# Kernel tuning notes

Hardware: AMD Instinct MI355X
Metric: run time of the kernel (lower is better)

## Reference

```python
import jax, jax.numpy as jnp
import numpy as np

B, T, IN, H, L = 8192, 200, 4, 16, 4
MLP_IN, MLP_HID, MLP_OUT = H * T, 64, IN * 7


def _lstm_layer(x, Wih, Whh, b):
    """x: [B,T,Din]; Wih: [4H,Din]; Whh: [4H,H]; b: [4H]. Returns [B,T,H].
    PyTorch gate order: i, f, g, o."""
    xg = jnp.einsum('btd,gd->btg', x, Wih) + b  # precompute input projections [B,T,4H]
    h0 = jnp.zeros((x.shape[0], H), x.dtype)
    c0 = jnp.zeros((x.shape[0], H), x.dtype)

    def step(carry, xt):
        h, c = carry
        gates = xt + h @ Whh.T  # [B,4H]
        i, f, g, o = jnp.split(gates, 4, axis=-1)
        i = jax.nn.sigmoid(i); f = jax.nn.sigmoid(f)
        g = jnp.tanh(g); o = jax.nn.sigmoid(o)
        c = f * c + i * g
        h = o * jnp.tanh(c)
        return (h, c), h

    _, hs = jax.lax.scan(step, (h0, c0), jnp.swapaxes(xg, 0, 1))  # [T,B,H]
    return jnp.swapaxes(hs, 0, 1)


def setup_inputs() -> dict:
    key = jax.random.key(0)
    ks = jax.random.split(key, 12)
    s = 1.0 / np.sqrt(H)
    u = lambda k, shp: jax.random.uniform(k, shp, jnp.float32, -s, s)
    x = jax.random.normal(ks[0], (B, T, IN), jnp.float32)
    Wih0 = u(ks[1], (4 * H, IN))            # layer 0 input weights
    Wih_rest = u(ks[2], (L - 1, 4 * H, H))  # layers 1..3
    Whh = u(ks[3], (L, 4 * H, H))
    bih = u(ks[4], (L, 4 * H))
    bhh = u(ks[5], (L, 4 * H))
    sm = 1.0 / np.sqrt(MLP_IN)
    W1 = jax.random.uniform(ks[6], (MLP_HID, MLP_IN), jnp.float32, -sm, sm)
    b1 = jax.random.uniform(ks[7], (MLP_HID,), jnp.float32, -sm, sm)
    sm2 = 1.0 / np.sqrt(MLP_HID)
    W2 = jax.random.uniform(ks[8], (MLP_OUT, MLP_HID), jnp.float32, -sm2, sm2)
    b2 = jax.random.uniform(ks[9], (MLP_OUT,), jnp.float32, -sm2, sm2)
    return {"x": x, "Wih0": Wih0, "Wih_rest": Wih_rest, "Whh": Whh,
            "bih": bih, "bhh": bhh, "W1": W1, "b1": b1, "W2": W2, "b2": b2}


def reference(x, Wih0, Wih_rest, Whh, bih, bhh, W1, b1, W2, b2):
    h = _lstm_layer(x, Wih0, Whh[0], bih[0] + bhh[0])
    for l in range(1, L):
        h = _lstm_layer(h, Wih_rest[l - 1], Whh[l], bih[l] + bhh[l])
    flat = h.reshape(-1, H * T)  # [B, 3200]
    hid = jax.nn.relu(flat @ W1.T + b1)
    return hid @ W2.T + b2  # [B, 28]
```

## Files before the change

### kernel.cpp

```cpp
#include <hip/hip_runtime.h>
#include <hip/hip_bf16.h>


typedef short  bf16x8 __attribute__((ext_vector_type(8)));
typedef float  f32x4  __attribute__((ext_vector_type(4)));

namespace {
constexpr int kT     = 200;
constexpr int kOut   = 28;
constexpr int kSteps = kT + 4;
constexpr float kNLog2e  = -1.4426950408889634f;
constexpr float kN2Log2e = -2.8853900817779268f;
constexpr int kW1Elems = 64 * 3200;
}

union FragU { bf16x8 v; unsigned u[4]; };

__device__ __forceinline__ float fast_rcp(float v){ return __builtin_amdgcn_rcpf(v); }
__device__ __forceinline__ float fast_exp2(float v){ return __builtin_amdgcn_exp2f(v); }
__device__ __forceinline__ float sig_scaled(float p){ return fast_rcp(1.0f + fast_exp2(p)); }
__device__ __forceinline__ float tanh_true(float v){
  return fmaf(fast_rcp(1.0f + fast_exp2(kN2Log2e*v)), 2.0f, -1.0f);
}

__device__ __forceinline__ void split8(const float* v, FragU& hi, FragU& lo){
#pragma unroll
  for (int r=0;r<4;++r){
    unsigned ua=__float_as_uint(v[2*r]), ub=__float_as_uint(v[2*r+1]);
    hi.u[r] = (ua>>16) | (ub & 0xffff0000u);
    float af=__uint_as_float(ua & 0xffff0000u);
    float bf=__uint_as_float(ub & 0xffff0000u);
    float al=v[2*r]-af, bl=v[2*r+1]-bf;
    lo.u[r] = (__float_as_uint(al)>>16) | (__float_as_uint(bl) & 0xffff0000u);
  }
}

__global__ __launch_bounds__(256)
void presplit_w1(const float* __restrict__ W1,
                 short* __restrict__ W1h, short* __restrict__ W1l){
  int i = blockIdx.x*256 + threadIdx.x;
  if (i < kW1Elems){
    float v = W1[i];
    unsigned u = __float_as_uint(v);
    float hif = __uint_as_float(u & 0xffff0000u);
    float lo  = v - hif;
    W1h[i] = (short)(u >> 16);
    W1l[i] = (short)(__float_as_uint(lo) >> 16);
  }
}

template<bool PS>
__global__ __launch_bounds__(256)
void lstm_pipe(const float* __restrict__ x,
               const float* __restrict__ Wih0,
               const float* __restrict__ Wihr,
               const float* __restrict__ Whh,
               const float* __restrict__ bih,
               const float* __restrict__ bhh,
               const float* __restrict__ W1,
               const float* __restrict__ b1,
               const float* __restrict__ W2,
               const float* __restrict__ b2,
               const short* __restrict__ W1h,
               const short* __restrict__ W1l,
               float* __restrict__ out)
{
  __shared__ float ldsH[2][4][16][16];
  __shared__ float ldsR[16][68];

  const int tid  = threadIdx.x;
  const int lane = tid & 63;
  const int wv   = tid >> 6;
  const int s    = lane & 15;
  const int q    = lane >> 4;
  const int l    = wv;
  const int sbase = blockIdx.x * 16;

  for (int i = tid; i < 2*4*16*16; i += 256) ((float*)ldsH)[i] = 0.f;

  FragU A[4][2];
#pragma unroll
  for (int tile=0;tile<4;++tile){
    const int grow = tile*16 + s;
    const float kE = (tile==2)? kN2Log2e : kNLog2e;
    float v[8];
    if (l==0){
#pragma unroll
      for (int e=0;e<8;++e){
        float w = 0.f;
        if (q==0 && e<4) w = Wih0[grow*4+e];
        if (q>=2)        w = Whh[grow*16 + (q&1)*8 + e];
        v[e] = w*kE;
      }
    } else {
#pragma unroll
      for (int e=0;e<8;++e){
        float w = (q<2) ? Wihr[((l-1)*64+grow)*16 + q*8 + e]
                        : Whh [(( l )*64+grow)*16 + (q&1)*8 + e];
        v[e] = w*kE;
      }
    }
    split8(v, A[tile][0], A[tile][1]);
  }

  f32x4 biasf[4];
#pragma unroll
  for (int tile=0;tile<4;++tile){
    const float kE = (tile==2)? kN2Log2e : kNLog2e;
#pragma unroll
    for (int r=0;r<4;++r){
      const int row = l*64 + tile*16 + 4*q + r;
      biasf[tile][r] = (bih[row] + bhh[row]) * kE;
    }
  }

  float cst[4] = {0.f,0.f,0.f,0.f};
  f32x4 mlpacc = (f32x4){0.f,0.f,0.f,0.f};
  float bufE[8];
#pragma unroll
  for (int e=0;e<8;++e) bufE[e]=0.f;

  const float* xp = x + (size_t)(sbase+s)*(kT*4);
  float4 xv_cur;
  if (l==0) xv_cur = *(const float4*)xp;

  const int rowW1 = wv*16 + s;
  const short* w1hp = W1h + (size_t)rowW1*3200;
  const short* w1lp = W1l + (size_t)rowW1*3200;
  const float* w1fp = W1  + (size_t)rowW1*3200;
  FragU  pWh, pWl;
  float4 pWa, pWb;

  __syncthreads();

  for (int n=0; n<kSteps; ++n){
    const int p = n & 1;
    const float (*rb)[16][16] = ldsH[p^1];
    float (*wb)[16][16] = ldsH[p];

    const int tm = n - 4;
    if (tm >= 0 && tm < kT && (tm&1)==0){
      const int off = 16*tm + q*8;
      if (PS){
        pWh.v = *(const bf16x8*)(w1hp + off);
        pWl.v = *(const bf16x8*)(w1lp + off);
      } else {
        pWa = *(const float4*)(w1fp + off);
        pWb = *(const float4*)(w1fp + off + 4);
      }
    }
    const int t = n - l;
    float4 xv_next;
    if (l==0 && t+1 < kT) xv_next = *(const float4*)(xp + 4*(t+1));

    if (t >= 0 && t < kT){
      float bv[8];
      {
        const int srcl = (q<2) ? ((l==0)?0:(l-1)) : l;
        const float* hp = &rb[srcl][s][(q&1)*8];
        const float4 h0 = *(const float4*)hp;
        const float4 h1 = *(const float4*)(hp+4);
        bv[0]=h0.x; bv[1]=h0.y; bv[2]=h0.z; bv[3]=h0.w;
        bv[4]=h1.x; bv[5]=h1.y; bv[6]=h1.z; bv[7]=h1.w;
      }
      if (l==0){
        if (q==0){
          bv[0]=xv_cur.x; bv[1]=xv_cur.y; bv[2]=xv_cur.z; bv[3]=xv_cur.w;
          bv[4]=0.f; bv[5]=0.f; bv[6]=0.f; bv[7]=0.f;
        } else if (q==1){
#pragma unroll
          for (int e=0;e<8;++e) bv[e]=0.f;
        }
      }
      FragU Bh,Bl; split8(bv,Bh,Bl);

      float si[4], sf[4], sg[4], so[4];
#pragma unroll
      for (int tile=0;tile<4;++tile){
        f32x4 acc = biasf[tile];
        acc = __builtin_amdgcn_mfma_f32_16x16x32_bf16(A[tile][0].v,Bh.v,acc,0,0,0);
        acc = __builtin_amdgcn_mfma_f32_16x16x32_bf16(A[tile][0].v,Bl.v,acc,0,0,0);
        acc = __builtin_amdgcn_mfma_f32_16x16x32_bf16(A[tile][1].v,Bh.v,acc,0,0,0);
#pragma unroll
        for (int r=0;r<4;++r){
          const float a = sig_scaled(acc[r]);
          if      (tile==0) si[r]=a;
          else if (tile==1) sf[r]=a;
          else if (tile==2) sg[r]=fmaf(a,2.f,-1.f);
          else              so[r]=a;
        }
      }
      float hn[4];
#pragma unroll
      for (int r=0;r<4;++r){
        cst[r] = fmaf(sf[r], cst[r], si[r]*sg[r]);
        hn[r] = so[r]*tanh_true(cst[r]);
      }
      f32x4 hv = (f32x4){hn[0],hn[1],hn[2],hn[3]};
      *(f32x4*)&wb[l][s][4*q] = hv;
    }
    if (l==0 && t+1 < kT) xv_cur = xv_next;

    if (tm >= 0 && tm < kT){
      const float* hp3 = &rb[3][s][(q&1)*8];
      const float4 h0 = *(const float4*)hp3;
      const float4 h1 = *(const float4*)(hp3+4);
      if ((tm & 1) == 0){
        bufE[0]=h0.x; bufE[1]=h0.y; bufE[2]=h0.z; bufE[3]=h0.w;
        bufE[4]=h1.x; bufE[5]=h1.y; bufE[6]=h1.z; bufE[7]=h1.w;
      } else {
        float bv[8];
        if (q<2){
#pragma unroll
          for (int e=0;e<8;++e) bv[e]=bufE[e];
        } else {
          bv[0]=h0.x; bv[1]=h0.y; bv[2]=h0.z; bv[3]=h0.w;
          bv[4]=h1.x; bv[5]=h1.y; bv[6]=h1.z; bv[7]=h1.w;
        }
        FragU Bh,Bl; split8(bv,Bh,Bl);
        FragU Ah,Al;
        if (PS){ Ah = pWh; Al = pWl; }
        else {
          float v[8] = {pWa.x,pWa.y,pWa.z,pWa.w,pWb.x,pWb.y,pWb.z,pWb.w};
          split8(v,Ah,Al);
        }
        mlpacc = __builtin_amdgcn_mfma_f32_16x16x32_bf16(Ah.v,Bh.v,mlpacc,0,0,0);
        mlpacc = __builtin_amdgcn_mfma_f32_16x16x32_bf16(Ah.v,Bl.v,mlpacc,0,0,0);
        mlpacc = __builtin_amdgcn_mfma_f32_16x16x32_bf16(Al.v,Bh.v,mlpacc,0,0,0);
      }
    }
    __syncthreads();
  }

  {
    f32x4 rv;
#pragma unroll
    for (int r=0;r<4;++r)
      rv[r] = fmaxf(mlpacc[r] + b1[wv*16 + 4*q + r], 0.f);
    *(f32x4*)&ldsR[s][wv*16 + 4*q] = rv;
  }
  __syncthreads();
  {
    const int o  = lane & 31;
    const int oc = (o < kOut) ? o : 0;
    float4 w2r[16];
#pragma unroll
    for (int c2=0;c2<16;++c2) w2r[c2] = *(const float4*)(W2 + oc*64 + 4*c2);
    const float bias2 = b2[oc];
#pragma unroll
    for (int mm=0;mm<2;++mm){
      const int s2 = wv*4 + 2*mm + (lane>>5);
      float a0=bias2, a1=0.f, a2=0.f, a3=0.f;
#pragma unroll
      for (int c2=0;c2<16;++c2){
        const float4 rvv = *(const float4*)&ldsR[s2][4*c2];
        a0 = fmaf(w2r[c2].x, rvv.x, a0);
        a1 = fmaf(w2r[c2].y, rvv.y, a1);
        a2 = fmaf(w2r[c2].z, rvv.z, a2);
        a3 = fmaf(w2r[c2].w, rvv.w, a3);
      }
      if (o < kOut) out[(size_t)(sbase+s2)*kOut + o] = (a0+a1)+(a2+a3);
    }
  }
}

extern "C" void kernel_launch(void* const* d_in, const int* in_sizes, int n_in,
                              void* d_out, int out_size, void* d_ws, size_t ws_size,
                              hipStream_t stream) {
  (void)in_sizes; (void)n_in; (void)out_size;
  const float* x    = (const float*)d_in[0];
  const float* Wih0 = (const float*)d_in[1];
  const float* Wihr = (const float*)d_in[2];
  const float* Whh  = (const float*)d_in[3];
  const float* bih  = (const float*)d_in[4];
  const float* bhh  = (const float*)d_in[5];
  const float* W1   = (const float*)d_in[6];
  const float* b1   = (const float*)d_in[7];
  const float* W2   = (const float*)d_in[8];
  const float* b2   = (const float*)d_in[9];
  float* out = (float*)d_out;

  const size_t splitBytes = (size_t)kW1Elems * sizeof(short) * 2;
  dim3 grid(8192/16), block(256);
  if (ws_size >= splitBytes) {
    short* W1h = (short*)d_ws;
    short* W1l = W1h + kW1Elems;
    hipLaunchKernelGGL(presplit_w1, dim3((kW1Elems+255)/256), dim3(256), 0, stream,
                       W1, W1h, W1l);
    hipLaunchKernelGGL(lstm_pipe<true>, grid, block, 0, stream,
                       x, Wih0, Wihr, Whh, bih, bhh, W1, b1, W2, b2, W1h, W1l, out);
  } else {
    hipLaunchKernelGGL(lstm_pipe<false>, grid, block, 0, stream,
                       x, Wih0, Wihr, Whh, bih, bhh, W1, b1, W2, b2,
                       (const short*)nullptr, (const short*)nullptr, out);
  }
}
```

Measured before the change: 330.3 us.

## Process two timesteps per pipeline stage to halve block barriers

The wavefront-per-layer pipeline now advances two timesteps per iteration. Each layer computes steps 2k and 2k+1 back to back, reading its own step-2k result from the write buffer. This halves the number of __syncthreads barriers and loop iterations, and the LDS buffers are padded to a stride of 20 floats. W1 fragments are prefetched one iteration ahead into separate current and next registers. The cost is longer serial work per wave between barriers and a little more register pressure.

```diff
diff --git a/kernel.cpp b/kernel.cpp
--- a/kernel.cpp
+++ b/kernel.cpp
@@ -8,7 +8,8 @@
 namespace {
 constexpr int kT     = 200;
 constexpr int kOut   = 28;
-constexpr int kSteps = kT + 4;
+constexpr int kPairs = kT / 2;
+constexpr int kSteps = kPairs + 4;
 constexpr float kNLog2e  = -1.4426950408889634f;
 constexpr float kN2Log2e = -2.8853900817779268f;
 constexpr int kW1Elems = 64 * 3200;
@@ -65,7 +66,7 @@
                const short* __restrict__ W1l,
                float* __restrict__ out)
 {
-  __shared__ float ldsH[2][4][16][16];
+  __shared__ float ldsH[2][4][2][16][20];
   __shared__ float ldsR[16][68];
 
   const int tid  = threadIdx.x;
@@ -74,9 +75,10 @@
   const int s    = lane & 15;
   const int q    = lane >> 4;
   const int l    = wv;
+  const int lm1  = (l==0) ? 0 : (l-1);
   const int sbase = blockIdx.x * 16;
 
-  for (int i = tid; i < 2*4*16*16; i += 256) ((float*)ldsH)[i] = 0.f;
+  for (int i = tid; i < 2*4*2*16*20; i += 256) ((float*)ldsH)[i] = 0.f;
 
   FragU A[4][2];
 #pragma unroll
@@ -116,112 +118,117 @@
 
   float cst[4] = {0.f,0.f,0.f,0.f};
   f32x4 mlpacc = (f32x4){0.f,0.f,0.f,0.f};
-  float bufE[8];
-#pragma unroll
-  for (int e=0;e<8;++e) bufE[e]=0.f;
 
   const float* xp = x + (size_t)(sbase+s)*(kT*4);
-  float4 xv_cur;
-  if (l==0) xv_cur = *(const float4*)xp;
+  float4 xA, xB;
+  if (l==0){
+    xA = *(const float4*)xp;
+    xB = *(const float4*)(xp+4);
+  }
 
   const int rowW1 = wv*16 + s;
   const short* w1hp = W1h + (size_t)rowW1*3200;
   const short* w1lp = W1l + (size_t)rowW1*3200;
   const float* w1fp = W1  + (size_t)rowW1*3200;
-  FragU  pWh, pWl;
-  float4 pWa, pWb;
+  FragU  pWhN, pWlN, pWhC, pWlC;
+  float4 pWaN, pWbN, pWaC, pWbC;
 
   __syncthreads();
 
   for (int n=0; n<kSteps; ++n){
     const int p = n & 1;
-    const float (*rb)[16][16] = ldsH[p^1];
-    float (*wb)[16][16] = ldsH[p];
-
-    const int tm = n - 4;
-    if (tm >= 0 && tm < kT && (tm&1)==0){
-      const int off = 16*tm + q*8;
-      if (PS){
-        pWh.v = *(const bf16x8*)(w1hp + off);
-        pWl.v = *(const bf16x8*)(w1lp + off);
-      } else {
-        pWa = *(const float4*)(w1fp + off);
-        pWb = *(const float4*)(w1fp + off + 4);
-      }
-    }
-    const int t = n - l;
-    float4 xv_next;
-    if (l==0 && t+1 < kT) xv_next = *(const float4*)(xp + 4*(t+1));
-
-    if (t >= 0 && t < kT){
-      float bv[8];
-      {
-        const int srcl = (q<2) ? ((l==0)?0:(l-1)) : l;
-        const float* hp = &rb[srcl][s][(q&1)*8];
-        const float4 h0 = *(const float4*)hp;
-        const float4 h1 = *(const float4*)(hp+4);
-        bv[0]=h0.x; bv[1]=h0.y; bv[2]=h0.z; bv[3]=h0.w;
-        bv[4]=h1.x; bv[5]=h1.y; bv[6]=h1.z; bv[7]=h1.w;
-      }
-      if (l==0){
-        if (q==0){
-          bv[0]=xv_cur.x; bv[1]=xv_cur.y; bv[2]=xv_cur.z; bv[3]=xv_cur.w;
-          bv[4]=0.f; bv[5]=0.f; bv[6]=0.f; bv[7]=0.f;
-        } else if (q==1){
-#pragma unroll
-          for (int e=0;e<8;++e) bv[e]=0.f;
-        }
-      }
-      FragU Bh,Bl; split8(bv,Bh,Bl);
-
-      float si[4], sf[4], sg[4], so[4];
-#pragma unroll
-      for (int tile=0;tile<4;++tile){
-        f32x4 acc = biasf[tile];
-        acc = __builtin_amdgcn_mfma_f32_16x16x32_bf16(A[tile][0].v,Bh.v,acc,0,0,0);
-        acc = __builtin_amdgcn_mfma_f32_16x16x32_bf16(A[tile][0].v,Bl.v,acc,0,0,0);
-        acc = __builtin_amdgcn_mfma_f32_16x16x32_bf16(A[tile][1].v,Bh.v,acc,0,0,0);
-#pragma unroll
-        for (int r=0;r<4;++r){
-          const float a = sig_scaled(acc[r]);
-          if      (tile==0) si[r]=a;
-          else if (tile==1) sf[r]=a;
-          else if (tile==2) sg[r]=fmaf(a,2.f,-1.f);
-          else              so[r]=a;
-        }
-      }
-      float hn[4];
-#pragma unroll
-      for (int r=0;r<4;++r){
-        cst[r] = fmaf(sf[r], cst[r], si[r]*sg[r]);
-        hn[r] = so[r]*tanh_true(cst[r]);
-      }
-      f32x4 hv = (f32x4){hn[0],hn[1],hn[2],hn[3]};
-      *(f32x4*)&wb[l][s][4*q] = hv;
-    }
-    if (l==0 && t+1 < kT) xv_cur = xv_next;
-
-    if (tm >= 0 && tm < kT){
-      const float* hp3 = &rb[3][s][(q&1)*8];
-      const float4 h0 = *(const float4*)hp3;
-      const float4 h1 = *(const float4*)(hp3+4);
-      if ((tm & 1) == 0){
-        bufE[0]=h0.x; bufE[1]=h0.y; bufE[2]=h0.z; bufE[3]=h0.w;
-        bufE[4]=h1.x; bufE[5]=h1.y; bufE[6]=h1.z; bufE[7]=h1.w;
-      } else {
+    float (*rb)[2][16][20] = ldsH[p^1];
+    float (*wb)[2][16][20] = ldsH[p];
+
+    {
+      const int mp = n - 3;
+      if (mp >= 0 && mp < kPairs){
+        const int off = 32*mp + q*8;
+        if (PS){
+          pWhN.v = *(const bf16x8*)(w1hp + off);
+          pWlN.v = *(const bf16x8*)(w1lp + off);
+        } else {
+          pWaN = *(const float4*)(w1fp + off);
+          pWbN = *(const float4*)(w1fp + off + 4);
+        }
+      }
+    }
+    const int pr = n - l;
+    float4 xnA, xnB;
+    if (l==0 && pr+1 < kPairs){
+      xnA = *(const float4*)(xp + 8*(pr+1));
+      xnB = *(const float4*)(xp + 8*(pr+1) + 4);
+    }
+
+    if (pr >= 0 && pr < kPairs){
+#pragma unroll
+      for (int st=0; st<2; ++st){
         float bv[8];
-        if (q<2){
-#pragma unroll
-          for (int e=0;e<8;++e) bv[e]=bufE[e];
-        } else {
+        {
+          const float* hp = (q < 2)
+            ? &rb[lm1][st][s][(q&1)*8]
+            : (st==0 ? &rb[l][1][s][(q&1)*8] : &wb[l][0][s][(q&1)*8]);
+          const float4 h0 = *(const float4*)hp;
+          const float4 h1 = *(const float4*)(hp+4);
           bv[0]=h0.x; bv[1]=h0.y; bv[2]=h0.z; bv[3]=h0.w;
           bv[4]=h1.x; bv[5]=h1.y; bv[6]=h1.z; bv[7]=h1.w;
         }
+        if (l==0){
+          if (q==0){
+            const float4 xv = st==0 ? xA : xB;
+            bv[0]=xv.x; bv[1]=xv.y; bv[2]=xv.z; bv[3]=xv.w;
+            bv[4]=0.f; bv[5]=0.f; bv[6]=0.f; bv[7]=0.f;
+          } else if (q==1){
+#pragma unroll
+            for (int e=0;e<8;++e) bv[e]=0.f;
+          }
+        }
+        FragU Bh,Bl; split8(bv,Bh,Bl);
+
+        float si[4], sf[4], sg[4], so[4];
+#pragma unroll
+        for (int tile=0;tile<4;++tile){
+          f32x4 acc = biasf[tile];
+          acc = __builtin_amdgcn_mfma_f32_16x16x32_bf16(A[tile][0].v,Bh.v,acc,0,0,0);
+          acc = __builtin_amdgcn_mfma_f32_16x16x32_bf16(A[tile][0].v,Bl.v,acc,0,0,0);
+          acc = __builtin_amdgcn_mfma_f32_16x16x32_bf16(A[tile][1].v,Bh.v,acc,0,0,0);
+#pragma unroll
+          for (int r=0;r<4;++r){
+            const float a = sig_scaled(acc[r]);
+            if      (tile==0) si[r]=a;
+            else if (tile==1) sf[r]=a;
+            else if (tile==2) sg[r]=fmaf(a,2.f,-1.f);
+            else              so[r]=a;
+          }
+        }
+        float hn[4];
+#pragma unroll
+        for (int r=0;r<4;++r){
+          cst[r] = fmaf(sf[r], cst[r], si[r]*sg[r]);
+          hn[r] = so[r]*tanh_true(cst[r]);
+        }
+        f32x4 hv = (f32x4){hn[0],hn[1],hn[2],hn[3]};
+        *(f32x4*)&wb[l][st][s][4*q] = hv;
+      }
+    }
+    if (l==0 && pr+1 < kPairs){ xA = xnA; xB = xnB; }
+
+    {
+      const int m = n - 4;
+      if (m >= 0 && m < kPairs){
+        float bv[8];
+        {
+          const float* hp3 = &rb[3][q>>1][s][(q&1)*8];
+          const float4 h0 = *(const float4*)hp3;
+          const float4 h1 = *(const float4*)(hp3+4);
+          bv[0]=h0.x; bv[1]=h0.y; bv[2]=h0.z; bv[3]=h0.w;
+          bv[4]=h1.x; bv[5]=h1.y; bv[6]=h1.z; bv[7]=h1.w;
+        }
         FragU Bh,Bl; split8(bv,Bh,Bl);
         FragU Ah,Al;
-        if (PS){ Ah = pWh; Al = pWl; }
+        if (PS){ Ah = pWhC; Al = pWlC; }
         else {
-          float v[8] = {pWa.x,pWa.y,pWa.z,pWa.w,pWb.x,pWb.y,pWb.z,pWb.w};
+          float v[8] = {pWaC.x,pWaC.y,pWaC.z,pWaC.w,pWbC.x,pWbC.y,pWbC.z,pWbC.w};
           split8(v,Ah,Al);
         }
         mlpacc = __builtin_amdgcn_mfma_f32_16x16x32_bf16(Ah.v,Bh.v,mlpacc,0,0,0);
@@ -229,6 +236,8 @@
         mlpacc = __builtin_amdgcn_mfma_f32_16x16x32_bf16(Al.v,Bh.v,mlpacc,0,0,0);
       }
     }
+    if (PS){ pWhC = pWhN; pWlC = pWlN; }
+    else   { pWaC = pWaN; pWbC = pWbN; }
     __syncthreads();
   }
 
```

Measured after the change: 293.4 us. -11.2%, faster.
